# Kernel optimization log

Hardware: AMD Instinct MI355X
Metric: run time of the kernel (lower is better)

The kernel has to match this reference:

```python
import jax, jax.numpy as jnp
import numpy as np

DIM = 1024
NUM_HEADS = 16
HEAD_DIM = DIM // NUM_HEADS
SCALE = HEAD_DIM ** -0.5
B, N = 4, 2048


def setup_inputs() -> dict:
    key = jax.random.key(0)
    kx, kq, kp = jax.random.split(key, 3)
    x = jax.random.normal(kx, (B, N, DIM), dtype=jnp.float32)
    # linear weights stored torch-style: [out_features, in_features]
    w_qkv = jax.random.normal(kq, (3 * DIM, DIM), dtype=jnp.float32) * (DIM ** -0.5)
    w_proj = jax.random.normal(kp, (DIM, DIM), dtype=jnp.float32) * (DIM ** -0.5)
    b_proj = jnp.zeros((DIM,), dtype=jnp.float32)
    return {"x": x, "w_qkv": w_qkv, "w_proj": w_proj, "b_proj": b_proj}


def reference(x, w_qkv, w_proj, b_proj):
    Bx, Nx, C = x.shape
    # qkv: [B,N,3C] -> [3,B,H,N,hd]
    qkv = x @ w_qkv.T
    qkv = qkv.reshape(Bx, Nx, 3, NUM_HEADS, C // NUM_HEADS).transpose(2, 0, 3, 1, 4)
    q, k, v = qkv[0], qkv[1], qkv[2]
    attn = jnp.einsum("bhqd,bhkd->bhqk", q, k) * SCALE
    attn = jax.nn.softmax(attn, axis=-1)
    out = jnp.einsum("bhqk,bhkd->bhqd", attn, v)  # [B,H,N,hd]
    out = out.transpose(0, 2, 1, 3).reshape(Bx, Nx, C)
    return out @ w_proj.T + b_proj
```

## Files before the change

kernel.cpp:

```cpp
#include <hip/hip_runtime.h>
#include <hip/hip_bf16.h>

typedef __bf16 bf16x8 __attribute__((ext_vector_type(8)));
typedef __bf16 bf16x4 __attribute__((ext_vector_type(4)));
typedef float  f32x4  __attribute__((ext_vector_type(4)));
typedef float  f32x16 __attribute__((ext_vector_type(16)));

#define DIM 1024
#define NHEAD 16
#define HD 64
#define BATCH 4
#define SEQ 2048
#define MROWS (BATCH * SEQ)
#define NX (MROWS * DIM)
#define NQW (3 * DIM * DIM)
#define NPW (DIM * DIM)

#define QSC (0.125f * 1.44269504088896340736f)

__global__ void cvt_all(const float* __restrict__ x, const float* __restrict__ wq,
                        const float* __restrict__ wp, __bf16* __restrict__ xb,
                        __bf16* __restrict__ wqb, __bf16* __restrict__ wpb) {
    const int total = (NX + NQW + NPW) / 4;
    int stride = gridDim.x * blockDim.x;
    for (int c = blockIdx.x * blockDim.x + threadIdx.x; c < total; c += stride) {
        int i = c * 4;
        const float* src; __bf16* dst; int off;
        if (i < NX)            { src = x;  dst = xb;  off = i; }
        else if (i < NX + NQW) { src = wq; dst = wqb; off = i - NX; }
        else                   { src = wp; dst = wpb; off = i - NX - NQW; }
        float4 v = *(const float4*)&src[off];
        bf16x4 o = { (__bf16)v.x, (__bf16)v.y, (__bf16)v.z, (__bf16)v.w };
        *(bf16x4*)&dst[off] = o;
    }
}

__global__ __launch_bounds__(256) void gemm_qkv(
    const __bf16* __restrict__ X, const __bf16* __restrict__ W,
    __bf16* __restrict__ Qo, __bf16* __restrict__ Ko, __bf16* __restrict__ Vt) {
    __shared__ __align__(16) __bf16 As[128][72];
    __shared__ __align__(16) __bf16 Bs[128][72];
    const int m0 = blockIdx.y * 128, n0 = blockIdx.x * 128;
    const int tid = threadIdx.x;
    const int w = tid >> 6, lane = tid & 63;
    const int wm = w >> 1, wn = w & 1;
    const int lr = lane & 15, lg = lane >> 4;
    const int ldr = tid >> 3;
    const int ldc = (tid & 7) * 8;

    f32x4 acc[4][4];
    const f32x4 z = {0.f, 0.f, 0.f, 0.f};
#pragma unroll
    for (int i = 0; i < 4; ++i)
#pragma unroll
        for (int j = 0; j < 4; ++j) acc[i][j] = z;

    for (int kt = 0; kt < DIM; kt += 64) {
#pragma unroll
        for (int rr = 0; rr < 128; rr += 32) {
            *(bf16x8*)&As[ldr + rr][ldc] =
                *(const bf16x8*)&X[(size_t)(m0 + ldr + rr) * DIM + kt + ldc];
            *(bf16x8*)&Bs[ldr + rr][ldc] =
                *(const bf16x8*)&W[(size_t)(n0 + ldr + rr) * DIM + kt + ldc];
        }
        __syncthreads();
#pragma unroll
        for (int kk = 0; kk < 2; ++kk) {
            bf16x8 a[4], b[4];
#pragma unroll
            for (int i = 0; i < 4; ++i)
                a[i] = *(const bf16x8*)&As[wm * 64 + i * 16 + lr][kk * 32 + lg * 8];
#pragma unroll
            for (int j = 0; j < 4; ++j)
                b[j] = *(const bf16x8*)&Bs[wn * 64 + j * 16 + lr][kk * 32 + lg * 8];
#pragma unroll
            for (int i = 0; i < 4; ++i)
#pragma unroll
                for (int j = 0; j < 4; ++j)
                    acc[i][j] = __builtin_amdgcn_mfma_f32_16x16x32_bf16(a[i], b[j], acc[i][j], 0, 0, 0);
        }
        __syncthreads();
    }

    const int t = n0 >> 10;
    if (t < 2) {
        __bf16* dst = (t == 0) ? Qo : Ko;
        const float sc = (t == 0) ? QSC : 1.0f;
#pragma unroll
        for (int i = 0; i < 4; ++i) {
#pragma unroll
            for (int j = 0; j < 4; ++j) {
                int n = n0 + wn * 64 + j * 16 + lr;
                int rem = n & 1023, h = rem >> 6, d = rem & 63;
#pragma unroll
                for (int rr = 0; rr < 4; ++rr) {
                    int m = m0 + wm * 64 + i * 16 + lg * 4 + rr;
                    int b = m >> 11, pos = m & 2047;
                    dst[(((size_t)b * NHEAD + h) * SEQ + pos) * HD + d] =
                        (__bf16)(acc[i][j][rr] * sc);
                }
            }
        }
    } else {
#pragma unroll
        for (int i = 0; i < 4; ++i) {
#pragma unroll
            for (int j = 0; j < 4; ++j) {
                int n = n0 + wn * 64 + j * 16 + lr;
                int rem = n & 1023, h = rem >> 6, d = rem & 63;
                int m = m0 + wm * 64 + i * 16 + lg * 4;
                int b = m >> 11, pos = m & 2047;
                bf16x4 v4 = { (__bf16)acc[i][j][0], (__bf16)acc[i][j][1],
                              (__bf16)acc[i][j][2], (__bf16)acc[i][j][3] };
                *(bf16x4*)&Vt[(((size_t)b * NHEAD + h) * HD + d) * SEQ + pos] = v4;
            }
        }
    }
}

__device__ __forceinline__ unsigned pk2(float a, float b) {
    __bf16 x = (__bf16)a, y = (__bf16)b;
    unsigned short xu = __builtin_bit_cast(unsigned short, x);
    unsigned short yu = __builtin_bit_cast(unsigned short, y);
    return (unsigned)xu | ((unsigned)yu << 16);
}

__global__ __launch_bounds__(256) void flash_attn6(
    const __bf16* __restrict__ Q, const __bf16* __restrict__ K,
    const __bf16* __restrict__ Vt, __bf16* __restrict__ AO) {
    __shared__ __align__(16) char ldsbuf[2][16384];
    const int L = blockIdx.x;
    const int xcd = L & 7;
    const int mloc = L >> 3;
    const int bh = xcd * 8 + (mloc >> 4);
    const int qt = mloc & 15;
    const int tid = threadIdx.x;
    const int w = tid >> 6, lane = tid & 63;
    const int l31 = lane & 31, hi = lane >> 5;
    const int qb = qt * 128 + w * 32;
    const size_t kvQ = (size_t)bh * SEQ * HD;
    const size_t kvV = (size_t)bh * HD * SEQ;

    bf16x8 qf[4];
#pragma unroll
    for (int ks = 0; ks < 4; ++ks)
        qf[ks] = *(const bf16x8*)&Q[kvQ + (size_t)(qb + l31) * HD + ks * 16 + hi * 8];

    bf16x8 ones;
#pragma unroll
    for (int j = 0; j < 8; ++j) ones[j] = (__bf16)1.0f;

    f32x16 o0 = {}, o1 = {}, lac = {};

    const char* gK = (const char*)K + kvQ * 2 + tid * 16;
    const char* gV = (const char*)Vt + kvV * 2 + (size_t)(tid >> 3) * 4096 + (tid & 7) * 16;
    const int dK = (tid & 7) * 1024 + (((tid >> 3) * 16) ^ ((tid & 7) * 16));
    const int dV = 8192 + dK;

    const int l31x16 = l31 * 16;
    const int hi1024 = hi * 1024;

#define PV_STEP(UARR, C, CT)                                                    \
    {                                                                           \
        unsigned w0_ = UARR[4 * C], w1_ = UARR[4 * C + 1];                      \
        unsigned w2_ = UARR[4 * C + 2], w3_ = UARR[4 * C + 3];                  \
        asm("v_permlane32_swap_b32 %0, %1" : "+v"(w0_), "+v"(w2_));             \
        asm("v_permlane32_swap_b32 %0, %1" : "+v"(w1_), "+v"(w3_));             \
        union { unsigned q[4]; bf16x8 v; } af_;                                 \
        af_.q[0] = w0_; af_.q[1] = w1_; af_.q[2] = w2_; af_.q[3] = w3_;         \
        int vx_ = 8192 + (CT) * 2048 + hi1024 + (l31x16 ^ ((2 * (CT) + hi) << 4)); \
        bf16x8 v0f = *(const bf16x8*)(ldb + vx_);                               \
        bf16x8 v1f = *(const bf16x8*)(ldb + vx_ + 512);                         \
        o0  = __builtin_amdgcn_mfma_f32_32x32x16_bf16(af_.v, v0f, o0, 0, 0, 0); \
        o1  = __builtin_amdgcn_mfma_f32_32x32x16_bf16(af_.v, v1f, o1, 0, 0, 0); \
        lac = __builtin_amdgcn_mfma_f32_32x32x16_bf16(af_.v, ones, lac, 0, 0, 0); \
    }

    const int NT = SEQ / 64;

    {
        uint4 a0 = *(const uint4*)(gK);
        uint4 a1 = *(const uint4*)(gK + 4096);
        uint4 a2 = *(const uint4*)(gV);
        uint4 a3 = *(const uint4*)(gV + 131072);
        gK += 8192; gV += 128;
        char* lb = &ldsbuf[0][0];
        *(uint4*)(lb + dK)       = a0;
        *(uint4*)(lb + dK + 512) = a1;
        *(uint4*)(lb + dV)       = a2;
        *(uint4*)(lb + dV + 512) = a3;
    }
    __syncthreads();

    int cur = 0;
    for (int t = 0; t < NT; ++t) {
        const bool pf = (t + 1 < NT);
        uint4 a0, a1, a2, a3;
        if (pf) {
            a0 = *(const uint4*)(gK);
            a1 = *(const uint4*)(gK + 4096);
            a2 = *(const uint4*)(gV);
            a3 = *(const uint4*)(gV + 131072);
            gK += 8192; gV += 128;
        }
        const char* ldb = &ldsbuf[cur][0];
        f32x16 s0 = {}, s1 = {};
#pragma unroll
        for (int ks = 0; ks < 4; ++ks) {
            int kx = ks * 2048 + hi1024 + (l31x16 ^ ((2 * ks + hi) << 4));
            bf16x8 k0f = *(const bf16x8*)(ldb + kx);
            bf16x8 k1f = *(const bf16x8*)(ldb + kx + 512);
            s0 = __builtin_amdgcn_mfma_f32_32x32x16_bf16(k0f, qf[ks], s0, 0, 0, 0);
            s1 = __builtin_amdgcn_mfma_f32_32x32x16_bf16(k1f, qf[ks], s1, 0, 0, 0);
        }
        unsigned u0[8], u1[8];
#pragma unroll
        for (int m2 = 0; m2 < 8; ++m2) {
            u0[m2] = pk2(__builtin_amdgcn_exp2f(s0[2 * m2]),
                         __builtin_amdgcn_exp2f(s0[2 * m2 + 1]));
            u1[m2] = pk2(__builtin_amdgcn_exp2f(s1[2 * m2]),
                         __builtin_amdgcn_exp2f(s1[2 * m2 + 1]));
        }
        PV_STEP(u0, 0, 0)
        PV_STEP(u0, 1, 1)
        PV_STEP(u1, 0, 2)
        PV_STEP(u1, 1, 3)
        if (pf) {
            char* lb = &ldsbuf[cur ^ 1][0];
            *(uint4*)(lb + dK)       = a0;
            *(uint4*)(lb + dK + 512) = a1;
            *(uint4*)(lb + dV)       = a2;
            *(uint4*)(lb + dV + 512) = a3;
        }
        __syncthreads();
        cur ^= 1;
    }
#undef PV_STEP

    const int b = bh >> 4, h = bh & 15;
#pragma unroll
    for (int r = 0; r < 16; ++r) {
        float inv = 1.0f / lac[r];
        int q = qb + (r & 3) + 8 * (r >> 2) + 4 * hi;
        size_t base = ((size_t)b * SEQ + q) * DIM + h * HD + l31;
        AO[base]      = (__bf16)(o0[r] * inv);
        AO[base + 32] = (__bf16)(o1[r] * inv);
    }
}

__global__ __launch_bounds__(256) void gemm_proj(
    const __bf16* __restrict__ A, const __bf16* __restrict__ W,
    const float* __restrict__ bias, float* __restrict__ out) {
    __shared__ __align__(16) __bf16 As[128][72];
    __shared__ __align__(16) __bf16 Bs[128][72];
    const int m0 = blockIdx.y * 128, n0 = blockIdx.x * 128;
    const int tid = threadIdx.x;
    const int w = tid >> 6, lane = tid & 63;
    const int wm = w >> 1, wn = w & 1;
    const int lr = lane & 15, lg = lane >> 4;
    const int ldr = tid >> 3;
    const int ldc = (tid & 7) * 8;

    f32x4 acc[4][4];
    const f32x4 z = {0.f, 0.f, 0.f, 0.f};
#pragma unroll
    for (int i = 0; i < 4; ++i)
#pragma unroll
        for (int j = 0; j < 4; ++j) acc[i][j] = z;

    for (int kt = 0; kt < DIM; kt += 64) {
#pragma unroll
        for (int rr = 0; rr < 128; rr += 32) {
            *(bf16x8*)&As[ldr + rr][ldc] =
                *(const bf16x8*)&A[(size_t)(m0 + ldr + rr) * DIM + kt + ldc];
            *(bf16x8*)&Bs[ldr + rr][ldc] =
                *(const bf16x8*)&W[(size_t)(n0 + ldr + rr) * DIM + kt + ldc];
        }
        __syncthreads();
#pragma unroll
        for (int kk = 0; kk < 2; ++kk) {
            bf16x8 a[4], b[4];
#pragma unroll
            for (int i = 0; i < 4; ++i)
                a[i] = *(const bf16x8*)&As[wm * 64 + i * 16 + lr][kk * 32 + lg * 8];
#pragma unroll
            for (int j = 0; j < 4; ++j)
                b[j] = *(const bf16x8*)&Bs[wn * 64 + j * 16 + lr][kk * 32 + lg * 8];
#pragma unroll
            for (int i = 0; i < 4; ++i)
#pragma unroll
                for (int j = 0; j < 4; ++j)
                    acc[i][j] = __builtin_amdgcn_mfma_f32_16x16x32_bf16(a[i], b[j], acc[i][j], 0, 0, 0);
        }
        __syncthreads();
    }

#pragma unroll
    for (int i = 0; i < 4; ++i) {
#pragma unroll
        for (int j = 0; j < 4; ++j) {
            int n = n0 + wn * 64 + j * 16 + lr;
            float bv = bias[n];
#pragma unroll
            for (int rr = 0; rr < 4; ++rr) {
                int m = m0 + wm * 64 + i * 16 + lg * 4 + rr;
                out[(size_t)m * DIM + n] = acc[i][j][rr] + bv;
            }
        }
    }
}

extern "C" void kernel_launch(void* const* d_in, const int* in_sizes, int n_in,
                              void* d_out, int out_size, void* d_ws, size_t ws_size,
                              hipStream_t stream) {
    const float* x    = (const float*)d_in[0];
    const float* wqkv = (const float*)d_in[1];
    const float* wproj= (const float*)d_in[2];
    const float* bproj= (const float*)d_in[3];
    float* out = (float*)d_out;

    __bf16* xb  = (__bf16*)d_ws;
    __bf16* wqb = xb + NX;
    __bf16* wpb = wqb + NQW;
    __bf16* Qb  = wpb + NPW;
    __bf16* Kb  = Qb + (size_t)NX;
    __bf16* Vtb = Kb + (size_t)NX;
    __bf16* AO  = xb;

    cvt_all<<<2048, 256, 0, stream>>>(x, wqkv, wproj, xb, wqb, wpb);
    gemm_qkv<<<dim3(24, 64), 256, 0, stream>>>(xb, wqb, Qb, Kb, Vtb);
    flash_attn6<<<1024, 256, 0, stream>>>(Qb, Kb, Vtb, AO);
    gemm_proj<<<dim3(8, 64), 256, 0, stream>>>(AO, wpb, bproj, out);
}
```

Before: 200.6 us.

## Double attention block size to 512 threads sharing each K/V tile

The flash attention kernel now runs 512 threads (8 waves) per block covering 256 query rows, instead of 256 threads covering 128. Each K/V tile loaded into shared memory is reused by twice as many waves, so each thread issues half as many global loads and LDS stores per tile, and half as many blocks reread the same K/V. The swizzled LDS read offsets are also precomputed into small per-thread arrays. The grid shrinks to 512 blocks, which may reduce occupancy and makes each block barrier wait on more waves.

```diff
diff --git a/kernel.cpp b/kernel.cpp
--- a/kernel.cpp
+++ b/kernel.cpp
@@ -125,19 +125,19 @@
     return (unsigned)xu | ((unsigned)yu << 16);
 }
 
-__global__ __launch_bounds__(256) void flash_attn6(
+__global__ __launch_bounds__(512) void flash_attn9(
     const __bf16* __restrict__ Q, const __bf16* __restrict__ K,
     const __bf16* __restrict__ Vt, __bf16* __restrict__ AO) {
     __shared__ __align__(16) char ldsbuf[2][16384];
     const int L = blockIdx.x;
     const int xcd = L & 7;
     const int mloc = L >> 3;
-    const int bh = xcd * 8 + (mloc >> 4);
-    const int qt = mloc & 15;
+    const int bh = xcd * 8 + (mloc >> 3);
+    const int qt = mloc & 7;
     const int tid = threadIdx.x;
     const int w = tid >> 6, lane = tid & 63;
     const int l31 = lane & 31, hi = lane >> 5;
-    const int qb = qt * 128 + w * 32;
+    const int qb = qt * 256 + w * 32;
     const size_t kvQ = (size_t)bh * SEQ * HD;
     const size_t kvV = (size_t)bh * HD * SEQ;
 
@@ -157,8 +157,12 @@
     const int dK = (tid & 7) * 1024 + (((tid >> 3) * 16) ^ ((tid & 7) * 16));
     const int dV = 8192 + dK;
 
-    const int l31x16 = l31 * 16;
-    const int hi1024 = hi * 1024;
+    int kxo[4], vxo[4];
+#pragma unroll
+    for (int i = 0; i < 4; ++i) {
+        kxo[i] = i * 2048 + hi * 1024 + ((l31 * 16) ^ ((2 * i + hi) << 4));
+        vxo[i] = 8192 + kxo[i];
+    }
 
 #define PV_STEP(UARR, C, CT)                                                    \
     {                                                                           \
@@ -168,9 +172,8 @@
         asm("v_permlane32_swap_b32 %0, %1" : "+v"(w1_), "+v"(w3_));             \
         union { unsigned q[4]; bf16x8 v; } af_;                                 \
         af_.q[0] = w0_; af_.q[1] = w1_; af_.q[2] = w2_; af_.q[3] = w3_;         \
-        int vx_ = 8192 + (CT) * 2048 + hi1024 + (l31x16 ^ ((2 * (CT) + hi) << 4)); \
-        bf16x8 v0f = *(const bf16x8*)(ldb + vx_);                               \
-        bf16x8 v1f = *(const bf16x8*)(ldb + vx_ + 512);                         \
+        bf16x8 v0f = *(const bf16x8*)(ldb + vxo[CT]);                           \
+        bf16x8 v1f = *(const bf16x8*)(ldb + vxo[CT] + 512);                     \
         o0  = __builtin_amdgcn_mfma_f32_32x32x16_bf16(af_.v, v0f, o0, 0, 0, 0); \
         o1  = __builtin_amdgcn_mfma_f32_32x32x16_bf16(af_.v, v1f, o1, 0, 0, 0); \
         lac = __builtin_amdgcn_mfma_f32_32x32x16_bf16(af_.v, ones, lac, 0, 0, 0); \
@@ -180,36 +183,29 @@
 
     {
         uint4 a0 = *(const uint4*)(gK);
-        uint4 a1 = *(const uint4*)(gK + 4096);
-        uint4 a2 = *(const uint4*)(gV);
-        uint4 a3 = *(const uint4*)(gV + 131072);
+        uint4 a1 = *(const uint4*)(gV);
         gK += 8192; gV += 128;
         char* lb = &ldsbuf[0][0];
-        *(uint4*)(lb + dK)       = a0;
-        *(uint4*)(lb + dK + 512) = a1;
-        *(uint4*)(lb + dV)       = a2;
-        *(uint4*)(lb + dV + 512) = a3;
+        *(uint4*)(lb + dK) = a0;
+        *(uint4*)(lb + dV) = a1;
     }
     __syncthreads();
 
     int cur = 0;
     for (int t = 0; t < NT; ++t) {
         const bool pf = (t + 1 < NT);
-        uint4 a0, a1, a2, a3;
+        uint4 a0, a1;
         if (pf) {
             a0 = *(const uint4*)(gK);
-            a1 = *(const uint4*)(gK + 4096);
-            a2 = *(const uint4*)(gV);
-            a3 = *(const uint4*)(gV + 131072);
+            a1 = *(const uint4*)(gV);
             gK += 8192; gV += 128;
         }
         const char* ldb = &ldsbuf[cur][0];
         f32x16 s0 = {}, s1 = {};
 #pragma unroll
         for (int ks = 0; ks < 4; ++ks) {
-            int kx = ks * 2048 + hi1024 + (l31x16 ^ ((2 * ks + hi) << 4));
-            bf16x8 k0f = *(const bf16x8*)(ldb + kx);
-            bf16x8 k1f = *(const bf16x8*)(ldb + kx + 512);
+            bf16x8 k0f = *(const bf16x8*)(ldb + kxo[ks]);
+            bf16x8 k1f = *(const bf16x8*)(ldb + kxo[ks] + 512);
             s0 = __builtin_amdgcn_mfma_f32_32x32x16_bf16(k0f, qf[ks], s0, 0, 0, 0);
             s1 = __builtin_amdgcn_mfma_f32_32x32x16_bf16(k1f, qf[ks], s1, 0, 0, 0);
         }
@@ -227,10 +223,8 @@
         PV_STEP(u1, 1, 3)
         if (pf) {
             char* lb = &ldsbuf[cur ^ 1][0];
-            *(uint4*)(lb + dK)       = a0;
-            *(uint4*)(lb + dK + 512) = a1;
-            *(uint4*)(lb + dV)       = a2;
-            *(uint4*)(lb + dV + 512) = a3;
+            *(uint4*)(lb + dK) = a0;
+            *(uint4*)(lb + dV) = a1;
         }
         __syncthreads();
         cur ^= 1;
@@ -329,6 +323,6 @@
 
     cvt_all<<<2048, 256, 0, stream>>>(x, wqkv, wproj, xb, wqb, wpb);
     gemm_qkv<<<dim3(24, 64), 256, 0, stream>>>(xb, wqb, Qb, Kb, Vtb);
-    flash_attn6<<<1024, 256, 0, stream>>>(Qb, Kb, Vtb, AO);
+    flash_attn9<<<512, 512, 0, stream>>>(Qb, Kb, Vtb, AO);
     gemm_proj<<<dim3(8, 64), 256, 0, stream>>>(AO, wpb, bproj, out);
 }
```

Measured after the change: 193.6 us. -3.5%, faster.
